# Optimization experiments

Measured on AMD Instinct MI355X. Metric: run time of the kernel, lower is better.

The kernel has to match this reference:

```python
import jax, jax.numpy as jnp
import numpy as np

B, N, C = 16, 1024, 256
SIZE = (512, 640)          # (H, W) image size
STRIDE = 8
H0, W0 = SIZE[0] // STRIDE, SIZE[1] // STRIDE   # 64, 80
P_TOK = H0 * W0                                  # 5120 base tokens
NHEAD, NLVL, NPTS = 8, 4, 4
HD = C // NHEAD
NUM_CLASSES = 7


def setup_inputs() -> dict:
    key = jax.random.key(0)
    ks = jax.random.split(key, 16)
    g = lambda k, shape, s=0.02: jax.random.normal(k, shape, jnp.float32) * s
    return {
        "q_t": jax.random.normal(ks[0], (B, N, C), jnp.float32),
        "h_t": jax.random.normal(ks[1], (B, P_TOK, C), jnp.float32),
        "p_head_t": jax.random.uniform(ks[2], (B, N, 2), jnp.float32)
                    * jnp.array([SIZE[1], SIZE[0]], jnp.float32),  # (x,y) in image coords
        "W_off": g(ks[3], (C, NHEAD * NLVL * NPTS * 2)),
        "b_off": g(ks[4], (NHEAD * NLVL * NPTS * 2,)),
        "W_attn": g(ks[5], (C, NHEAD * NLVL * NPTS)),
        "b_attn": g(ks[6], (NHEAD * NLVL * NPTS,)),
        "W_v": g(ks[7], (C, C)), "b_v": g(ks[8], (C,)),
        "W_o": g(ks[9], (C, C)), "b_o": g(ks[10], (C,)),
        "W_p1": g(ks[11], (2 * C, C)), "b_p1": g(ks[12], (C,)),
        "W_p2": g(ks[13], (C, NUM_CLASSES)), "b_p2": g(ks[14], (NUM_CLASSES,)),
    }


def _bilinear_sample(value_l, loc):
    """value_l: (B,Hl,Wl,nh,hd); loc: (B,N,nh,NPTS,2) in [0,1] normalized (x,y).
    grid_sample semantics: align_corners=False, padding_mode='zeros'.
    Returns (B,nh,N,NPTS,hd)."""
    Bb, Hl, Wl = value_l.shape[0], value_l.shape[1], value_l.shape[2]
    x = loc[..., 0] * Wl - 0.5
    y = loc[..., 1] * Hl - 0.5
    x0 = jnp.floor(x); y0 = jnp.floor(y)
    wx = x - x0; wy = y - y0
    x0i = x0.astype(jnp.int32); y0i = y0.astype(jnp.int32)
    flat = value_l.reshape(Bb, Hl * Wl, NHEAD, HD).transpose(0, 2, 1, 3)  # (B,nh,S,hd)

    def corner(xi, yi):
        valid = ((xi >= 0) & (xi < Wl) & (yi >= 0) & (yi < Hl)).astype(value_l.dtype)
        idx = (jnp.clip(yi, 0, Hl - 1) * Wl + jnp.clip(xi, 0, Wl - 1)).transpose(0, 2, 1, 3)  # (B,nh,N,P)
        g = jnp.take_along_axis(flat, idx.reshape(Bb, NHEAD, -1)[..., None], axis=2)
        g = g.reshape(Bb, NHEAD, idx.shape[2], idx.shape[3], HD)
        return g * valid.transpose(0, 2, 1, 3)[..., None]

    tw = lambda w: w.transpose(0, 2, 1, 3)[..., None]  # (B,nh,N,P,1)
    return (corner(x0i, y0i) * tw((1 - wx) * (1 - wy))
            + corner(x0i + 1, y0i) * tw(wx * (1 - wy))
            + corner(x0i, y0i + 1) * tw((1 - wx) * wy)
            + corner(x0i + 1, y0i + 1) * tw(wx * wy))


def reference(q_t, h_t, p_head_t, W_off, b_off, W_attn, b_attn,
              W_v, b_v, W_o, b_o, W_p1, b_p1, W_p2, b_p2):
    # normalize point predictions to [0,1] (x by W, y by H)
    p_norm = jnp.clip(p_head_t / jnp.array([SIZE[1], SIZE[0]], jnp.float32), 0.0, 1.0)

    # ---- get_deformable_inputs: 4-level pyramid by 2x2 average pooling ----
    cur = h_t.reshape(B, H0, W0, C)
    feats, shapes = [], []
    for l in range(NLVL):
        feats.append(cur)
        shapes.append((cur.shape[1], cur.shape[2]))
        if l < NLVL - 1:
            h, w = cur.shape[1], cur.shape[2]
            cur = cur.reshape(B, h // 2, 2, w // 2, 2, C).mean(axis=(2, 4))
    f_scales = jnp.concatenate([f.reshape(B, -1, C) for f in feats], axis=1)  # (B,S,C)

    # ---- DMSMHA_Block (multi-scale deformable attention) ----
    value = (f_scales @ W_v + b_v).reshape(B, -1, NHEAD, HD)
    offsets = (q_t @ W_off + b_off).reshape(B, N, NHEAD, NLVL, NPTS, 2)
    attn = jax.nn.softmax(
        (q_t @ W_attn + b_attn).reshape(B, N, NHEAD, NLVL * NPTS), axis=-1
    ).reshape(B, N, NHEAD, NLVL, NPTS)

    out = jnp.zeros((B, NHEAD, N, HD), jnp.float32)
    start = 0
    for l, (Hl, Wl) in enumerate(shapes):
        Sl = Hl * Wl
        vl = value[:, start:start + Sl].reshape(B, Hl, Wl, NHEAD, HD)
        start += Sl
        norm = jnp.array([Wl, Hl], jnp.float32)
        loc = p_norm[:, :, None, None, :] + offsets[:, :, :, l] / norm  # (B,N,nh,P,2)
        sampled = _bilinear_sample(vl, loc)                              # (B,nh,N,P,hd)
        w = attn[:, :, :, l].transpose(0, 2, 1, 3)                       # (B,nh,N,P)
        out = out + jnp.einsum('bhnp,bhnpd->bhnd', w, sampled)

    q_local = out.transpose(0, 2, 1, 3).reshape(B, N, C) @ W_o + b_o

    # ---- fuse + MLP head ----
    q_fused = jnp.concatenate([q_t, q_local], axis=-1)
    hid = jax.nn.relu(q_fused @ W_p1 + b_p1)
    logits = hid @ W_p2 + b_p2   # (B,N,num_classes)
    return logits
```

## Files before the change

### kernel.cpp

```cpp
#include <hip/hip_runtime.h>
#include <math.h>


namespace {

constexpr int kB = 16;
constexpr int kN = 1024;
constexpr int kC = 256;
constexpr int kNCLS = 7;
constexpr int kSTOT = 6800;

typedef __attribute__((ext_vector_type(8))) short short8;
typedef __attribute__((ext_vector_type(4))) float f32x4;

__device__ inline ushort f2bf(float f) {
  union { float f; unsigned u; } v; v.f = f;
  unsigned r = (v.u + 0x7fffu + ((v.u >> 16) & 1u)) >> 16;
  return (ushort)r;
}
__device__ inline float bf2f(ushort h) {
  union { unsigned u; float f; } v; v.u = ((unsigned)h) << 16;
  return v.f;
}

__device__ inline void gload16(const ushort* g, ushort* l) {
  __builtin_amdgcn_global_load_lds(
      (const __attribute__((address_space(1))) void*)g,
      (__attribute__((address_space(3))) void*)l, 16, 0, 0);
}

__global__ void cast_f2b_kernel(const float* __restrict__ in, ushort* __restrict__ out, int n4) {
  int i = blockIdx.x * 256 + threadIdx.x;
  if (i >= n4) return;
  float4 v = ((const float4*)in)[i];
  ((ushort4*)out)[i] = make_ushort4(f2bf(v.x), f2bf(v.y), f2bf(v.z), f2bf(v.w));
}

__global__ void pool_b2b_kernel(const ushort* __restrict__ fin, ushort* __restrict__ fout,
                                int oh, int ow, int so_in, int so_out) {
  int idx = blockIdx.x * 256 + threadIdx.x;
  if (idx >= kB * oh * ow * kC) return;
  int c = idx & 255; int t = idx >> 8;
  int x = t % ow; t /= ow; int y = t % oh; int b = t / oh;
  int iw = ow * 2;
  const ushort* p = fin + (((size_t)b * kSTOT + so_in + y * 2 * iw + x * 2) << 8) + c;
  float s = 0.25f * (bf2f(p[0]) + bf2f(p[256]) + bf2f(p[iw * 256]) + bf2f(p[iw * 256 + 256]));
  fout[(((size_t)b * kSTOT + so_out + y * ow + x) << 8) + c] = f2bf(s);
}

__global__ void wtrans_all_kernel(const float* __restrict__ s0, const float* __restrict__ s1,
                                  const float* __restrict__ s2, const float* __restrict__ s3,
                                  const float* __restrict__ s4,
                                  ushort* __restrict__ d0, ushort* __restrict__ d1,
                                  ushort* __restrict__ d2, ushort* __restrict__ d3,
                                  ushort* __restrict__ d4) {
  __shared__ float t[32][33];
  const float* W; ushort* Wt; int K, N;
  switch (blockIdx.z) {
    case 0: W = s0; Wt = d0; K = 256; N = 256; break;
    case 1: W = s1; Wt = d1; K = 256; N = 256; break;
    case 2: W = s2; Wt = d2; K = 256; N = 128; break;
    case 3: W = s3; Wt = d3; K = 256; N = 256; break;
    default: W = s4; Wt = d4; K = 512; N = 256; break;
  }
  int nx = blockIdx.x << 5, ky = blockIdx.y << 5;
  if (nx >= N || ky >= K) return;
  int lx = threadIdx.x & 31, ly = threadIdx.x >> 5;
#pragma unroll
  for (int i = 0; i < 32; i += 8)
    t[ly + i][lx] = W[(size_t)(ky + ly + i) * N + nx + lx];
  __syncthreads();
#pragma unroll
  for (int i = 0; i < 32; i += 8)
    Wt[(size_t)(nx + ly + i) * K + ky + lx] = f2bf(t[lx][ly + i]);
}

template <int KTOT, bool SPLITK, int OMODE, bool RELU>
__global__ __launch_bounds__(256) void gemm_bf16_kernel(
    const ushort* __restrict__ A, const ushort* __restrict__ A2,
    const ushort* __restrict__ Wt, const float* __restrict__ bias,
    const float* __restrict__ bias2, void* __restrict__ Cout,
    void* __restrict__ Cout2, int ldc) {
  __shared__ ushort Asm[2][128 * 32];
  __shared__ ushort Bsm[2][128 * 32];
  const int tid = threadIdx.x;
  const int w = tid >> 6, l = tid & 63;
  const int bm = blockIdx.y << 7, bn = blockIdx.x << 7;
  const int wm = w >> 1, wn = w & 1;

  const int c0 = w * 2, c1 = w * 2 + 1;
  const int G0 = c0 * 64 + l, G1 = c1 * 64 + l;
  const int r0 = G0 >> 2, g0 = G0 & 3;
  const int r1 = G1 >> 2, g1 = G1 & 3;
  const int sz0 = (g0 ^ ((r0 >> 1) & 3)) << 3;
  const int sz1 = (g1 ^ ((r1 >> 1) & 3)) << 3;
  const int ak = SPLITK ? 256 : KTOT;
  const ushort* sA0 = A + (size_t)(bm + r0) * ak + sz0;
  const ushort* sA1 = A + (size_t)(bm + r1) * ak + sz1;
  const ushort* sA0b = SPLITK ? A2 + (size_t)(bm + r0) * 256 + sz0 : nullptr;
  const ushort* sA1b = SPLITK ? A2 + (size_t)(bm + r1) * 256 + sz1 : nullptr;
  const ushort* sB0 = Wt + (size_t)(bn + r0) * KTOT + sz0;
  const ushort* sB1 = Wt + (size_t)(bn + r1) * KTOT + sz1;

  const int e = l >> 4, rl = l & 15;
  int aoff[4], boff[4];
#pragma unroll
  for (int i = 0; i < 4; ++i) {
    int r = wm * 64 + i * 16 + rl;
    aoff[i] = r * 32 + ((e ^ ((r >> 1) & 3)) << 3);
    int rb = wn * 64 + i * 16 + rl;
    boff[i] = rb * 32 + ((e ^ ((rb >> 1) & 3)) << 3);
  }

  f32x4 acc[4][4];
#pragma unroll
  for (int i = 0; i < 4; ++i)
#pragma unroll
    for (int j = 0; j < 4; ++j) acc[i][j] = (f32x4){0.f, 0.f, 0.f, 0.f};

  auto stage = [&](int buf, int k0) {
    const ushort *a0, *a1;
    if (SPLITK && k0 >= 256) {
      a0 = sA0b + (k0 - 256);
      a1 = sA1b + (k0 - 256);
    } else {
      a0 = sA0 + k0;
      a1 = sA1 + k0;
    }
    gload16(a0, &Asm[buf][c0 * 512]);
    gload16(a1, &Asm[buf][c1 * 512]);
    gload16(sB0 + k0, &Bsm[buf][c0 * 512]);
    gload16(sB1 + k0, &Bsm[buf][c1 * 512]);
  };

  constexpr int nt = KTOT / 32;
  stage(0, 0);
  __syncthreads();
  for (int t = 0; t < nt; ++t) {
    const int cur = t & 1;
    if (t + 1 < nt) stage(cur ^ 1, (t + 1) * 32);
    short8 af[4], bfr[4];
#pragma unroll
    for (int i = 0; i < 4; ++i) af[i] = *(const short8*)&Asm[cur][aoff[i]];
#pragma unroll
    for (int j = 0; j < 4; ++j) bfr[j] = *(const short8*)&Bsm[cur][boff[j]];
#pragma unroll
    for (int i = 0; i < 4; ++i)
#pragma unroll
      for (int j = 0; j < 4; ++j)
        acc[i][j] = __builtin_amdgcn_mfma_f32_16x16x32_bf16(bfr[j], af[i], acc[i][j], 0, 0, 0);
    __syncthreads();
  }

#pragma unroll
  for (int j = 0; j < 4; ++j) {
    int ch = bn + wn * 64 + j * 16 + e * 4;
    float4 b4;
    if (OMODE == 2)
      b4 = (ch < 256) ? *(const float4*)(bias + ch) : *(const float4*)(bias2 + ch - 256);
    else
      b4 = *(const float4*)(bias + ch);
    float bv[4] = {b4.x, b4.y, b4.z, b4.w};
#pragma unroll
    for (int i = 0; i < 4; ++i) {
      int sp = bm + wm * 64 + i * 16 + rl;
      float v[4];
#pragma unroll
      for (int r = 0; r < 4; ++r) {
        v[r] = acc[i][j][r] + bv[r];
        if (RELU) v[r] = fmaxf(v[r], 0.f);
      }
      if (OMODE == 0) {
        *(float4*)&((float*)Cout)[(size_t)sp * ldc + ch] = make_float4(v[0], v[1], v[2], v[3]);
      } else if (OMODE == 1) {
        *(ushort4*)&((ushort*)Cout)[(size_t)sp * ldc + ch] =
            make_ushort4(f2bf(v[0]), f2bf(v[1]), f2bf(v[2]), f2bf(v[3]));
      } else {
        if (ch < 256)
          *(float4*)&((float*)Cout)[(size_t)sp * 256 + ch] = make_float4(v[0], v[1], v[2], v[3]);
        else
          *(float4*)&((float*)Cout2)[(size_t)sp * 128 + (ch - 256)] =
              make_float4(v[0], v[1], v[2], v[3]);
      }
    }
  }
}

__global__ __launch_bounds__(256) void gemm_f32a_kernel(
    const float* __restrict__ A, const ushort* __restrict__ Wt,
    const float* __restrict__ bias, ushort* __restrict__ Cout) {
  __shared__ ushort Asm[2][128 * 32];
  __shared__ ushort Bsm[2][128 * 32];
  const int tid = threadIdx.x;
  const int w = tid >> 6, l = tid & 63;
  const int by = blockIdx.y;
  const int bn = blockIdx.x << 7;
  const int bm = by << 7;
  const int wm = w >> 1, wn = w & 1;

  const int ar = tid >> 1, ah = tid & 1;
  const float* aSrc = A + (size_t)(bm + ar) * 256 + ah * 16;
  const int s_ar = (ar >> 1) & 3;
  const int ad0 = ar * 32 + (((2 * ah + 0) ^ s_ar) << 3);
  const int ad1 = ar * 32 + (((2 * ah + 1) ^ s_ar) << 3);

  const int c0 = w * 2, c1 = w * 2 + 1;
  const int G0 = c0 * 64 + l, G1 = c1 * 64 + l;
  const int r0 = G0 >> 2, g0 = G0 & 3;
  const int r1 = G1 >> 2, g1 = G1 & 3;
  const ushort* sB0 = Wt + (size_t)(bn + r0) * 256 + ((g0 ^ ((r0 >> 1) & 3)) << 3);
  const ushort* sB1 = Wt + (size_t)(bn + r1) * 256 + ((g1 ^ ((r1 >> 1) & 3)) << 3);

  const int e = l >> 4, rl = l & 15;
  int aoff[4], boff[4];
#pragma unroll
  for (int i = 0; i < 4; ++i) {
    int r = wm * 64 + i * 16 + rl;
    aoff[i] = r * 32 + ((e ^ ((r >> 1) & 3)) << 3);
    int rb = wn * 64 + i * 16 + rl;
    boff[i] = rb * 32 + ((e ^ ((rb >> 1) & 3)) << 3);
  }

  f32x4 acc[4][4];
#pragma unroll
  for (int i = 0; i < 4; ++i)
#pragma unroll
    for (int j = 0; j < 4; ++j) acc[i][j] = (f32x4){0.f, 0.f, 0.f, 0.f};

  float4 av[4];
  auto loadA = [&](int k0) {
#pragma unroll
    for (int q = 0; q < 4; ++q) av[q] = *(const float4*)(aSrc + k0 + 4 * q);
  };
  auto writeA = [&](int buf) {
    ushort u[16];
#pragma unroll
    for (int q = 0; q < 4; ++q) {
      u[4 * q + 0] = f2bf(av[q].x);
      u[4 * q + 1] = f2bf(av[q].y);
      u[4 * q + 2] = f2bf(av[q].z);
      u[4 * q + 3] = f2bf(av[q].w);
    }
    *(short8*)&Asm[buf][ad0] =
        (short8){(short)u[0], (short)u[1], (short)u[2], (short)u[3],
                 (short)u[4], (short)u[5], (short)u[6], (short)u[7]};
    *(short8*)&Asm[buf][ad1] =
        (short8){(short)u[8], (short)u[9], (short)u[10], (short)u[11],
                 (short)u[12], (short)u[13], (short)u[14], (short)u[15]};
  };
  auto stageB = [&](int buf, int k0) {
    gload16(sB0 + k0, &Bsm[buf][c0 * 512]);
    gload16(sB1 + k0, &Bsm[buf][c1 * 512]);
  };

  loadA(0);
  stageB(0, 0);
  writeA(0);
  __syncthreads();
  for (int t = 0; t < 8; ++t) {
    const int cur = t & 1;
    if (t < 7) {
      loadA((t + 1) * 32);
      stageB(cur ^ 1, (t + 1) * 32);
    }
    short8 af[4], bfr[4];
#pragma unroll
    for (int i = 0; i < 4; ++i) af[i] = *(const short8*)&Asm[cur][aoff[i]];
#pragma unroll
    for (int j = 0; j < 4; ++j) bfr[j] = *(const short8*)&Bsm[cur][boff[j]];
#pragma unroll
    for (int i = 0; i < 4; ++i)
#pragma unroll
      for (int j = 0; j < 4; ++j)
        acc[i][j] = __builtin_amdgcn_mfma_f32_16x16x32_bf16(bfr[j], af[i], acc[i][j], 0, 0, 0);
    if (t < 7) writeA(cur ^ 1);
    __syncthreads();
  }

  const int b = by / 40;
  const int sb = (by - b * 40) << 7;
  ushort* outB = Cout + (((size_t)(b * 6800 + sb)) << 8);
#pragma unroll
  for (int j = 0; j < 4; ++j) {
    int ch = bn + wn * 64 + j * 16 + e * 4;
    float4 b4 = *(const float4*)(bias + ch);
    float bv[4] = {b4.x, b4.y, b4.z, b4.w};
#pragma unroll
    for (int i = 0; i < 4; ++i) {
      int sp = wm * 64 + i * 16 + rl;
      float v[4];
#pragma unroll
      for (int r = 0; r < 4; ++r) v[r] = acc[i][j][r] + bv[r];
      *(ushort4*)&outB[(size_t)sp * 256 + ch] =
          make_ushort4(f2bf(v[0]), f2bf(v[1]), f2bf(v[2]), f2bf(v[3]));
    }
  }
}

__global__ void deform_kernel(
    const ushort* __restrict__ value, const float* __restrict__ off,
    const float* __restrict__ attnl, const float* __restrict__ p_head,
    ushort* __restrict__ samp) {
  int blk = (int)blockIdx.x;
  int sw = (blk & 7) * 256 + (blk >> 3);
  int wvi = (sw << 2) + (threadIdx.x >> 6);
  int l = threadIdx.x & 63;
  int nq = l >> 5;
  int lh = l & 31;
  int h = lh >> 2;
  int pt = wvi * 2 + nq;
  int b = pt >> 10;
  size_t bn = (size_t)pt;

  float ph = (lh < 2) ? p_head[bn * 2 + lh] : 0.f;
  float px = __shfl(ph, (nq << 5) + 0, 64) * (1.0f / 640.0f);
  float py = __shfl(ph, (nq << 5) + 1, 64) * (1.0f / 512.0f);
  px = fminf(fmaxf(px, 0.f), 1.f);
  py = fminf(fmaxf(py, 0.f), 1.f);

  const float4* offp = (const float4*)(off + (bn << 8));
  float4 ofv0 = offp[2 * lh];
  float4 ofv1 = offp[2 * lh + 1];
  float4 atv = ((const float4*)(attnl + (bn << 7)))[lh];

  float m = fmaxf(fmaxf(atv.x, atv.y), fmaxf(atv.z, atv.w));
  m = fmaxf(m, __shfl_xor(m, 1, 64));
  m = fmaxf(m, __shfl_xor(m, 2, 64));
  float e0 = expf(atv.x - m), e1 = expf(atv.y - m);
  float e2 = expf(atv.z - m), e3 = expf(atv.w - m);
  float s = e0 + e1 + e2 + e3;
  s += __shfl_xor(s, 1, 64);
  s += __shfl_xor(s, 2, 64);
  float inv = 1.f / s;
  atv = make_float4(e0 * inv, e1 * inv, e2 * inv, e3 * inv);

  float acc[8];
#pragma unroll
  for (int i = 0; i < 8; ++i) acc[i] = 0.f;
  const ushort* vbb = value + (((size_t)b * kSTOT) << 8) + (lh << 3);

#pragma unroll 1
  for (int lv = 0; lv < 4; ++lv) {
    const int Wl = 80 >> lv, Hl = 64 >> lv;
    const int offL = (lv == 0) ? 0 : (lv == 1) ? 5120 : (lv == 2) ? 6400 : 6720;
    const ushort* vb = vbb + (((size_t)offL) << 8);
    const int src = (nq << 5) + (h << 2) + lv;
    const float fx = px * (float)Wl - 0.5f;
    const float fy = py * (float)Hl - 0.5f;
#pragma unroll
    for (int pp = 0; pp < 4; ++pp) {
      float sx, sy;
      if ((pp >> 1) == 0) {
        sx = (pp & 1) ? ofv0.z : ofv0.x;
        sy = (pp & 1) ? ofv0.w : ofv0.y;
      } else {
        sx = (pp & 1) ? ofv1.z : ofv1.x;
        sy = (pp & 1) ? ofv1.w : ofv1.y;
      }
      float ox = __shfl(sx, src, 64);
      float oy = __shfl(sy, src, 64);
      float sa = pp == 0 ? atv.x : pp == 1 ? atv.y : pp == 2 ? atv.z : atv.w;
      float aw = __shfl(sa, src, 64);

      float xx = fx + ox;
      float yy = fy + oy;
      float x0f = floorf(xx), y0f = floorf(yy);
      float wx = xx - x0f, wy = yy - y0f;
      int x0 = (int)x0f, y0 = (int)y0f;
      float w00 = (1.f - wx) * (1.f - wy) * aw;
      float w01 = wx * (1.f - wy) * aw;
      float w10 = (1.f - wx) * wy * aw;
      float w11 = wx * wy * aw;
      auto corner = [&](int xi, int yi, float wgt) {
        bool valid = (xi >= 0) && (xi < Wl) && (yi >= 0) && (yi < Hl);
        int xc = xi < 0 ? 0 : (xi > Wl - 1 ? Wl - 1 : xi);
        int yc = yi < 0 ? 0 : (yi > Hl - 1 ? Hl - 1 : yi);
        short8 d = *(const short8*)(vb + (((size_t)(yc * Wl + xc)) << 8));
        float wg = valid ? wgt : 0.f;
#pragma unroll
        for (int i = 0; i < 8; ++i) acc[i] = fmaf(wg, bf2f((ushort)d[i]), acc[i]);
      };
      corner(x0, y0, w00);
      corner(x0 + 1, y0, w01);
      corner(x0, y0 + 1, w10);
      corner(x0 + 1, y0 + 1, w11);
    }
  }
  ushort o[8];
#pragma unroll
  for (int i = 0; i < 8; ++i) o[i] = f2bf(acc[i]);
  *(short8*)(samp + (bn << 8) + (lh << 3)) =
      (short8){(short)o[0], (short)o[1], (short)o[2], (short)o[3],
               (short)o[4], (short)o[5], (short)o[6], (short)o[7]};
}

__global__ void head_kernel(const float* __restrict__ hid, const float* __restrict__ W2,
                            const float* __restrict__ b2, float* __restrict__ outp) {
  int gid = blockIdx.x * 256 + threadIdx.x;
  int wave = gid >> 6;
  int lane = threadIdx.x & 63;
  if (wave >= kB * kN) return;
  const float* hrow = hid + ((size_t)wave << 8);
  float acc[kNCLS];
#pragma unroll
  for (int j = 0; j < kNCLS; ++j) acc[j] = 0.f;
  for (int k = lane; k < kC; k += 64) {
    float hv = hrow[k];
    const float* wr = W2 + k * kNCLS;
#pragma unroll
    for (int j = 0; j < kNCLS; ++j) acc[j] = fmaf(hv, wr[j], acc[j]);
  }
#pragma unroll
  for (int m = 32; m > 0; m >>= 1) {
#pragma unroll
    for (int j = 0; j < kNCLS; ++j) acc[j] += __shfl_xor(acc[j], m);
  }
  float r = 0.f;
#pragma unroll
  for (int j = 0; j < kNCLS; ++j)
    if (lane == j) r = acc[j] + b2[j];
  if (lane < kNCLS) outp[(size_t)wave * kNCLS + lane] = r;
}

}

extern "C" void kernel_launch(void* const* d_in, const int* in_sizes, int n_in,
                              void* d_out, int out_size, void* d_ws, size_t ws_size,
                              hipStream_t stream) {
  const float* q_t    = (const float*)d_in[0];
  const float* h_t    = (const float*)d_in[1];
  const float* p_head = (const float*)d_in[2];
  const float* W_off  = (const float*)d_in[3];
  const float* b_off  = (const float*)d_in[4];
  const float* W_attn = (const float*)d_in[5];
  const float* b_attn = (const float*)d_in[6];
  const float* W_v    = (const float*)d_in[7];
  const float* b_v    = (const float*)d_in[8];
  const float* W_o    = (const float*)d_in[9];
  const float* b_o    = (const float*)d_in[10];
  const float* W_p1   = (const float*)d_in[11];
  const float* b_p1   = (const float*)d_in[12];
  const float* W_p2   = (const float*)d_in[13];
  const float* b_p2   = (const float*)d_in[14];
  float* out = (float*)d_out;
  char* wsb = (char*)d_ws;

  ushort* value = (ushort*)(wsb + 55705600);
  ushort* q_bf  = (ushort*)(wsb + 111411200);
  float*  offb  = (float*)(wsb + 119799808);
  float*  attnl = (float*)(wsb + 136577024);
  ushort* samp  = (ushort*)(wsb + 144965632);
  ushort* qloc  = (ushort*)(wsb + 153354240);
  float*  hid   = (float*)(wsb + 161742848);
  ushort* wtp   = (ushort*)(wsb + 178520064);
  ushort* Wt_v  = wtp;
  ushort* Wt_oa = wtp + 65536;
  ushort* Wt_o  = wtp + 163840;
  ushort* Wt_p1 = wtp + 229376;

  cast_f2b_kernel<<<4096, 256, 0, stream>>>(q_t, q_bf, kB * kN * 64);

  wtrans_all_kernel<<<dim3(8, 16, 5), 256, 0, stream>>>(
      W_v, W_off, W_attn, W_o, W_p1,
      Wt_v, Wt_oa, Wt_oa + 65536, Wt_o, Wt_p1);

  gemm_f32a_kernel<<<dim3(2, 640), 256, 0, stream>>>(h_t, Wt_v, b_v, value);

  pool_b2b_kernel<<<20480, 256, 0, stream>>>(value, value, 32, 40, 0, 5120);
  pool_b2b_kernel<<<5120, 256, 0, stream>>>(value, value, 16, 20, 5120, 6400);
  pool_b2b_kernel<<<1280, 256, 0, stream>>>(value, value, 8, 10, 6400, 6720);

  gemm_bf16_kernel<256, false, 2, false><<<dim3(3, 128), 256, 0, stream>>>(
      q_bf, nullptr, Wt_oa, b_off, b_attn, offb, attnl, 256);

  deform_kernel<<<2048, 256, 0, stream>>>(value, offb, attnl, p_head, samp);

  gemm_bf16_kernel<256, false, 1, false><<<dim3(2, 128), 256, 0, stream>>>(
      samp, nullptr, Wt_o, b_o, nullptr, qloc, nullptr, 256);

  gemm_bf16_kernel<512, true, 0, true><<<dim3(2, 128), 256, 0, stream>>>(
      q_bf, qloc, Wt_p1, b_p1, nullptr, hid, nullptr, 256);

  head_kernel<<<4096, 256, 0, stream>>>(hid, W_p2, b_p2, out);
}
```

Measured before the change: 152.1 us.

## Fold W_o into W_p1 and deepen A-prefetch pipeline in f32 GEMM

Precomputes a combined weight W_o·W_p1[256:] and a folded bias in a new small kernel. This removes the separate q_local projection GEMM, so the MLP GEMM reads the sampled features directly. Separately, the fp32-A value-projection GEMM now prefetches A two K-steps ahead using even/odd register sets, with explicit vmcnt/lgkmcnt waits and raw s_barrier in place of __syncthreads. Folding the weights in bf16 changes rounding slightly, and the manual waitcnt scheduling is fragile.

```diff
diff --git a/kernel.cpp b/kernel.cpp
--- a/kernel.cpp
+++ b/kernel.cpp
@@ -12,6 +12,9 @@
 
 typedef __attribute__((ext_vector_type(8))) short short8;
 typedef __attribute__((ext_vector_type(4))) float f32x4;
+
+#define VM_WAIT(n) asm volatile("s_waitcnt vmcnt(" #n ")" ::: "memory")
+#define LGKM_WAIT0 asm volatile("s_waitcnt lgkmcnt(0)" ::: "memory")
 
 __device__ inline ushort f2bf(float f) {
   union { float f; unsigned u; } v; v.f = f;
@@ -73,6 +76,30 @@
 #pragma unroll
   for (int i = 0; i < 32; i += 8)
     Wt[(size_t)(nx + ly + i) * K + ky + lx] = f2bf(t[lx][ly + i]);
+}
+
+__global__ void wcomb_kernel(const float* __restrict__ W_o, const float* __restrict__ W_p1,
+                             const float* __restrict__ b_o, const float* __restrict__ b_p1,
+                             const ushort* __restrict__ Wt_p1,
+                             ushort* __restrict__ Wt_p1c, float* __restrict__ bp1c) {
+  __shared__ float wcol[256];
+  __shared__ float wsum[4];
+  int h = blockIdx.x;
+  int in = threadIdx.x;
+  wcol[in] = W_p1[(size_t)(256 + in) * 256 + h];
+  __syncthreads();
+  float s = 0.f;
+  const float* wo = W_o + (size_t)in * 256;
+#pragma unroll 4
+  for (int out = 0; out < 256; ++out) s = fmaf(wo[out], wcol[out], s);
+  Wt_p1c[(size_t)h * 512 + 256 + in] = f2bf(s);
+  Wt_p1c[(size_t)h * 512 + in] = Wt_p1[(size_t)h * 512 + in];
+  float part = b_o[in] * wcol[in];
+#pragma unroll
+  for (int m = 32; m > 0; m >>= 1) part += __shfl_xor(part, m);
+  if ((in & 63) == 0) wsum[in >> 6] = part;
+  __syncthreads();
+  if (in == 0) bp1c[h] = b_p1[h] + wsum[0] + wsum[1] + wsum[2] + wsum[3];
 }
 
 template <int KTOT, bool SPLITK, int OMODE, bool RELU>
@@ -227,41 +254,65 @@
 #pragma unroll
     for (int j = 0; j < 4; ++j) acc[i][j] = (f32x4){0.f, 0.f, 0.f, 0.f};
 
-  float4 av[4];
-  auto loadA = [&](int k0) {
-#pragma unroll
-    for (int q = 0; q < 4; ++q) av[q] = *(const float4*)(aSrc + k0 + 4 * q);
+  float4 avE[4], avO[4];
+  auto loadE = [&](int k0) {
+#pragma unroll
+    for (int q = 0; q < 4; ++q) avE[q] = *(const float4*)(aSrc + k0 + 4 * q);
   };
-  auto writeA = [&](int buf) {
+  auto loadO = [&](int k0) {
+#pragma unroll
+    for (int q = 0; q < 4; ++q) avO[q] = *(const float4*)(aSrc + k0 + 4 * q);
+  };
+  auto writeE = [&](int buf) {
     ushort u[16];
 #pragma unroll
     for (int q = 0; q < 4; ++q) {
-      u[4 * q + 0] = f2bf(av[q].x);
-      u[4 * q + 1] = f2bf(av[q].y);
-      u[4 * q + 2] = f2bf(av[q].z);
-      u[4 * q + 3] = f2bf(av[q].w);
-    }
-    *(short8*)&Asm[buf][ad0] =
-        (short8){(short)u[0], (short)u[1], (short)u[2], (short)u[3],
-                 (short)u[4], (short)u[5], (short)u[6], (short)u[7]};
-    *(short8*)&Asm[buf][ad1] =
-        (short8){(short)u[8], (short)u[9], (short)u[10], (short)u[11],
-                 (short)u[12], (short)u[13], (short)u[14], (short)u[15]};
+      u[4 * q] = f2bf(avE[q].x); u[4 * q + 1] = f2bf(avE[q].y);
+      u[4 * q + 2] = f2bf(avE[q].z); u[4 * q + 3] = f2bf(avE[q].w);
+    }
+    *(short8*)&Asm[buf][ad0] = (short8){(short)u[0], (short)u[1], (short)u[2], (short)u[3],
+                                        (short)u[4], (short)u[5], (short)u[6], (short)u[7]};
+    *(short8*)&Asm[buf][ad1] = (short8){(short)u[8], (short)u[9], (short)u[10], (short)u[11],
+                                        (short)u[12], (short)u[13], (short)u[14], (short)u[15]};
+  };
+  auto writeO = [&](int buf) {
+    ushort u[16];
+#pragma unroll
+    for (int q = 0; q < 4; ++q) {
+      u[4 * q] = f2bf(avO[q].x); u[4 * q + 1] = f2bf(avO[q].y);
+      u[4 * q + 2] = f2bf(avO[q].z); u[4 * q + 3] = f2bf(avO[q].w);
+    }
+    *(short8*)&Asm[buf][ad0] = (short8){(short)u[0], (short)u[1], (short)u[2], (short)u[3],
+                                        (short)u[4], (short)u[5], (short)u[6], (short)u[7]};
+    *(short8*)&Asm[buf][ad1] = (short8){(short)u[8], (short)u[9], (short)u[10], (short)u[11],
+                                        (short)u[12], (short)u[13], (short)u[14], (short)u[15]};
   };
   auto stageB = [&](int buf, int k0) {
     gload16(sB0 + k0, &Bsm[buf][c0 * 512]);
     gload16(sB1 + k0, &Bsm[buf][c1 * 512]);
   };
 
-  loadA(0);
   stageB(0, 0);
-  writeA(0);
-  __syncthreads();
+  __builtin_amdgcn_sched_barrier(0);
+  loadE(0);
+  loadO(32);
+  VM_WAIT(4);
+  writeE(0);
+  LGKM_WAIT0;
+  __builtin_amdgcn_sched_barrier(0);
+  __builtin_amdgcn_s_barrier();
+  __builtin_amdgcn_sched_barrier(0);
+
+#pragma unroll
   for (int t = 0; t < 8; ++t) {
     const int cur = t & 1;
     if (t < 7) {
-      loadA((t + 1) * 32);
       stageB(cur ^ 1, (t + 1) * 32);
+      __builtin_amdgcn_sched_barrier(0);
+    }
+    if (t < 6) {
+      if ((t & 1) == 0) loadE((t + 2) * 32);
+      else              loadO((t + 2) * 32);
     }
     short8 af[4], bfr[4];
 #pragma unroll
@@ -273,8 +324,22 @@
 #pragma unroll
       for (int j = 0; j < 4; ++j)
         acc[i][j] = __builtin_amdgcn_mfma_f32_16x16x32_bf16(bfr[j], af[i], acc[i][j], 0, 0, 0);
-    if (t < 7) writeA(cur ^ 1);
-    __syncthreads();
+    if (t < 6) {
+      VM_WAIT(6);
+      if ((t & 1) == 0) writeO(cur ^ 1); else writeE(cur ^ 1);
+      VM_WAIT(4);
+      LGKM_WAIT0;
+    } else if (t == 6) {
+      VM_WAIT(2);
+      writeO(cur ^ 1);
+      VM_WAIT(0);
+      LGKM_WAIT0;
+    }
+    if (t < 7) {
+      __builtin_amdgcn_sched_barrier(0);
+      __builtin_amdgcn_s_barrier();
+      __builtin_amdgcn_sched_barrier(0);
+    }
   }
 
   const int b = by / 40;
@@ -450,13 +515,14 @@
   float*  offb  = (float*)(wsb + 119799808);
   float*  attnl = (float*)(wsb + 136577024);
   ushort* samp  = (ushort*)(wsb + 144965632);
-  ushort* qloc  = (ushort*)(wsb + 153354240);
   float*  hid   = (float*)(wsb + 161742848);
   ushort* wtp   = (ushort*)(wsb + 178520064);
-  ushort* Wt_v  = wtp;
-  ushort* Wt_oa = wtp + 65536;
-  ushort* Wt_o  = wtp + 163840;
-  ushort* Wt_p1 = wtp + 229376;
+  ushort* Wt_v   = wtp;
+  ushort* Wt_oa  = wtp + 65536;
+  ushort* Wt_o   = wtp + 163840;
+  ushort* Wt_p1  = wtp + 229376;
+  ushort* Wt_p1c = wtp + 360448;
+  float*  bp1c   = (float*)(wtp + 491520);
 
   cast_f2b_kernel<<<4096, 256, 0, stream>>>(q_t, q_bf, kB * kN * 64);
 
@@ -464,6 +530,8 @@
       W_v, W_off, W_attn, W_o, W_p1,
       Wt_v, Wt_oa, Wt_oa + 65536, Wt_o, Wt_p1);
 
+  wcomb_kernel<<<256, 256, 0, stream>>>(W_o, W_p1, b_o, b_p1, Wt_p1, Wt_p1c, bp1c);
+
   gemm_f32a_kernel<<<dim3(2, 640), 256, 0, stream>>>(h_t, Wt_v, b_v, value);
 
   pool_b2b_kernel<<<20480, 256, 0, stream>>>(value, value, 32, 40, 0, 5120);
@@ -475,11 +543,8 @@
 
   deform_kernel<<<2048, 256, 0, stream>>>(value, offb, attnl, p_head, samp);
 
-  gemm_bf16_kernel<256, false, 1, false><<<dim3(2, 128), 256, 0, stream>>>(
-      samp, nullptr, Wt_o, b_o, nullptr, qloc, nullptr, 256);
-
   gemm_bf16_kernel<512, true, 0, true><<<dim3(2, 128), 256, 0, stream>>>(
-      q_bf, qloc, Wt_p1, b_p1, nullptr, hid, nullptr, 256);
+      q_bf, samp, Wt_p1c, bp1c, nullptr, hid, nullptr, 256);
 
   head_kernel<<<4096, 256, 0, stream>>>(hid, W_p2, b_p2, out);
 }
```

Result: slower. 157.4 us (+3.4%).
